# Kernel tuning notes

Measured on AMD Instinct MI355X. Metric: run time of the kernel, lower is better.

Reference implementation:

```python
import jax, jax.numpy as jnp
import numpy as np

DIM = 2048
NUM_HEADS = 16
HEAD_DIM = DIM // NUM_HEADS  # 128
B, T = 2, 2048
ROPE_BASE = 10000.0


def _rope_tables(seq_len, head_dim, dtype=jnp.float32):
    inv_freq = 1.0 / (ROPE_BASE ** (jnp.arange(0, head_dim, 2, dtype=jnp.float32) / head_dim))
    t = jnp.arange(seq_len, dtype=jnp.float32)
    freqs = jnp.einsum('i,j->ij', t, inv_freq)          # [T, head_dim/2]
    emb = jnp.concatenate([freqs, freqs], axis=-1)       # [T, head_dim]
    return jnp.cos(emb).astype(dtype), jnp.sin(emb).astype(dtype)


def _rotate_half(x):
    x1, x2 = jnp.split(x, 2, axis=-1)
    return jnp.concatenate([-x2, x1], axis=-1)


def setup_inputs() -> dict:
    key = jax.random.key(0)
    k1, k2, k3 = jax.random.split(key, 3)
    x = jax.random.normal(k1, (B, T, DIM), dtype=jnp.float32)
    w_qkv = jax.random.normal(k2, (3 * DIM, DIM), dtype=jnp.float32) * (DIM ** -0.5)
    w_out = jax.random.normal(k3, (DIM, DIM), dtype=jnp.float32) * (DIM ** -0.5)
    return {"x": x, "w_qkv": w_qkv, "w_out": w_out}


def reference(x, w_qkv, w_out):
    b, t, _ = x.shape
    scale = HEAD_DIM ** -0.5

    qkv = x @ w_qkv.T                                    # [B, T, 3*dim]
    q, k, v = jnp.split(qkv, 3, axis=-1)
    # [B, H, T, hd]
    q = q.reshape(b, t, NUM_HEADS, HEAD_DIM).transpose(0, 2, 1, 3)
    k = k.reshape(b, t, NUM_HEADS, HEAD_DIM).transpose(0, 2, 1, 3)
    v = v.reshape(b, t, NUM_HEADS, HEAD_DIM).transpose(0, 2, 1, 3)

    cos, sin = _rope_tables(t, HEAD_DIM, x.dtype)        # [T, hd] broadcast over B,H
    q = q * cos + _rotate_half(q) * sin
    k = k * cos + _rotate_half(k) * sin

    scores = jnp.einsum('bhqd,bhkd->bhqk', q, k) * scale  # [B, H, T, T]
    causal = jnp.tril(jnp.ones((t, t), dtype=bool))
    scores = jnp.where(causal, scores, jnp.float32(-jnp.inf).astype(scores.dtype))
    attn = jax.nn.softmax(scores, axis=-1)
    out = jnp.einsum('bhqk,bhkd->bhqd', attn, v)         # [B, H, T, hd]
    out = out.transpose(0, 2, 1, 3).reshape(b, t, DIM)
    out = out @ w_out.T
    return out
```

## Files before the change

### kernel.cpp

```cpp
#include <hip/hip_runtime.h>
#include <hip/hip_bf16.h>
#include <stdint.h>
#include <math.h>

#define DIMC 2048
#define NH 16
#define HD 128
#define BBATCH 2
#define TSEQ 2048
#define MROWS (BBATCH*TSEQ)
#define NQKV (3*DIMC)

typedef __attribute__((ext_vector_type(8))) short short8;
typedef __attribute__((ext_vector_type(4))) float f32x4;

#define BAR() asm volatile("s_barrier" ::: "memory")

__device__ __forceinline__ short f2bf(float f) {
  union { float f; uint32_t u; } v; v.f = f;
  uint32_t r = (v.u + 0x7fffu + ((v.u >> 16) & 1u)) >> 16;
  return (short)(uint16_t)r;
}
__device__ __forceinline__ float bf2f(short s) {
  union { uint32_t u; float f; } v; v.u = ((uint32_t)(uint16_t)s) << 16;
  return v.f;
}
__device__ __forceinline__ void g2lds16(const void* g, void* l) {
  __builtin_amdgcn_global_load_lds((const __attribute__((address_space(1))) void*)g,
                                   (__attribute__((address_space(3))) void*)l, 16, 0, 0);
}

__global__ void rope_tables(float* __restrict__ cos_t, float* __restrict__ sin_t) {
  int idx = blockIdx.x * blockDim.x + threadIdx.x;
  int t = idx >> 6, j = idx & 63;
  double inv = exp(-((double)(2 * j) / 128.0) * log(10000.0));
  float fr = (float)t * (float)inv;
  cos_t[idx] = cosf(fr);
  sin_t[idx] = sinf(fr);
}

__global__ void cast_f32_bf16(const float* __restrict__ in, short* __restrict__ out, int n8) {
  int i = blockIdx.x * blockDim.x + threadIdx.x;
  if (i >= n8) return;
  const float4* p = (const float4*)in;
  float4 a = p[2 * i], b = p[2 * i + 1];
  short8 o;
  o[0] = f2bf(a.x); o[1] = f2bf(a.y); o[2] = f2bf(a.z); o[3] = f2bf(a.w);
  o[4] = f2bf(b.x); o[5] = f2bf(b.y); o[6] = f2bf(b.z); o[7] = f2bf(b.w);
  ((short8*)out)[i] = o;
}

__global__ void rope_apply(short* __restrict__ q, short* __restrict__ k,
                           const float* __restrict__ cos_t, const float* __restrict__ sin_t) {
  int idx = blockIdx.x * blockDim.x + threadIdx.x;
  int j = idx & 63;
  int t = (idx >> 6) & (TSEQ - 1);
  int bh = idx >> 17;
  size_t base = ((size_t)bh * TSEQ + t) * HD;
  float c = cos_t[t * 64 + j], s = sin_t[t * 64 + j];
  float x1 = bf2f(q[base + j]), x2 = bf2f(q[base + j + 64]);
  q[base + j]      = f2bf(x1 * c - x2 * s);
  q[base + j + 64] = f2bf(x2 * c + x1 * s);
  float y1 = bf2f(k[base + j]), y2 = bf2f(k[base + j + 64]);
  k[base + j]      = f2bf(y1 * c - y2 * s);
  k[base + j + 64] = f2bf(y2 * c + y1 * s);
}

__device__ __forceinline__ void stage128(short* lds_base, const short* gsrc, int ldg, int tid) {
  #pragma unroll
  for (int j = 0; j < 2; ++j) {
    int L = j * 512 + tid;
    int r = L >> 3, pc = L & 7;
    g2lds16(gsrc + (size_t)r * ldg + ((pc ^ (r & 7)) << 3), lds_base + L * 8);
  }
}
__device__ __forceinline__ short8 ldsfrag(const short* base, int row, int c) {
  return *(const short8*)(base + row * 64 + ((c ^ (row & 7)) << 3));
}

template<int EPI>
__global__ __launch_bounds__(512, 2)
void gemm256(const short* __restrict__ A, const short* __restrict__ B,
             int M, int N, int K,
             float* __restrict__ Cout,
             short* __restrict__ qp, short* __restrict__ kp, short* __restrict__ vp) {
  __shared__ short Ab[2][256 * 64];
  __shared__ short Bb[3][128 * 64];
  const int tid = threadIdx.x;
  const int lane = tid & 63, wave = tid >> 6;
  const int wm = wave >> 2, wn = wave & 3;
  const int bn = blockIdx.x, bm = blockIdx.y;
  const int rowA0 = bm * 256, rowB0 = bn * 128;
  const int NT = K / 64;
  const int l15 = lane & 15, l4 = lane >> 4;
  f32x4 acc[8][2] = {};

  stage128(&Ab[0][0],        A + (size_t)rowA0 * K,         K, tid);
  stage128(&Ab[0][128 * 64], A + (size_t)(rowA0 + 128) * K, K, tid);
  stage128(&Bb[0][0],        B + (size_t)rowB0 * K,         K, tid);
  stage128(&Bb[1][0],        B + (size_t)rowB0 * K + 64,    K, tid);
  asm volatile("s_waitcnt vmcnt(2)" ::: "memory");
  BAR();

  for (int t = 0; t < NT; ++t) {
    const short* At = Ab[t & 1];
    const short* Bt = Bb[t % 3];
    short* Anx = Ab[(t + 1) & 1];
    short* Bnx = Bb[(t + 2) % 3];
    const short* Ag = A + (size_t)rowA0 * K + (t + 1) * 64;
    const short* Bg = B + (size_t)rowB0 * K + (t + 2) * 64;
    short8 bfrag[2][2];
    #pragma unroll
    for (int ph = 0; ph < 4; ++ph) {
      short8 afrag[2][2];
      if (ph == 0) {
        #pragma unroll
        for (int n = 0; n < 2; ++n)
          #pragma unroll
          for (int ks = 0; ks < 2; ++ks)
            bfrag[n][ks] = ldsfrag(Bt, wn * 32 + n * 16 + l15, ks * 4 + l4);
      }
      #pragma unroll
      for (int m2 = 0; m2 < 2; ++m2)
        #pragma unroll
        for (int ks = 0; ks < 2; ++ks)
          afrag[m2][ks] = ldsfrag(At, wm * 128 + (ph * 2 + m2) * 16 + l15, ks * 4 + l4);
      if (ph == 0 && t + 1 < NT) stage128(Anx,            Ag,                    K, tid);
      if (ph == 1 && t + 1 < NT) stage128(Anx + 128 * 64, Ag + (size_t)128 * K,  K, tid);
      if (ph == 2 && t + 2 < NT) stage128(Bnx,            Bg,                    K, tid);
      if (ph == 3) {
        if (t + 2 < NT) asm volatile("s_waitcnt vmcnt(2)" ::: "memory");
        else            asm volatile("s_waitcnt vmcnt(0)" ::: "memory");
      }
      BAR();
      __builtin_amdgcn_s_setprio(1);
      #pragma unroll
      for (int m2 = 0; m2 < 2; ++m2)
        #pragma unroll
        for (int n = 0; n < 2; ++n)
          #pragma unroll
          for (int ks = 0; ks < 2; ++ks)
            acc[ph * 2 + m2][n] =
                __builtin_amdgcn_mfma_f32_16x16x32_bf16(afrag[m2][ks], bfrag[n][ks],
                                                        acc[ph * 2 + m2][n], 0, 0, 0);
      __builtin_amdgcn_s_setprio(0);
    }
  }

  if (EPI == 1) {
    #pragma unroll
    for (int m = 0; m < 8; ++m)
      #pragma unroll
      for (int n = 0; n < 2; ++n)
        #pragma unroll
        for (int i = 0; i < 4; ++i) {
          int gm = rowA0 + wm * 128 + m * 16 + (l4 << 2) + i;
          int gn = rowB0 + wn * 32 + n * 16 + l15;
          Cout[(size_t)gm * N + gn] = acc[m][n][i];
        }
  } else {
    short* dst = (bn < 16) ? qp : (bn < 32) ? kp : vp;
    int h = bn & 15;
    #pragma unroll
    for (int m = 0; m < 8; ++m)
      #pragma unroll
      for (int n = 0; n < 2; ++n)
        #pragma unroll
        for (int i = 0; i < 4; ++i) {
          int gm = rowA0 + wm * 128 + m * 16 + (l4 << 2) + i;
          int b = gm >> 11, tt = gm & 2047;
          int d = wn * 32 + n * 16 + l15;
          dst[(((size_t)b * NH + h) * TSEQ + tt) * HD + d] = f2bf(acc[m][n][i]);
        }
  }
}

__global__ __launch_bounds__(256)
void flash_attn(const short* __restrict__ Q, const short* __restrict__ K,
                const short* __restrict__ V, short* __restrict__ Oout) {
  __shared__ short Ks[64 * 128];
  __shared__ short Vt[128 * 64];
  __shared__ short Pl[4 * 16 * 64];
  int tid = threadIdx.x, lane = tid & 63, wave = tid >> 6;
  int bid = blockIdx.x;
  int qt = (TSEQ / 64 - 1) - (bid >> 5);
  int hb = bid & 31;
  int h = hb & 15, b = hb >> 4;
  size_t bh_off = ((size_t)b * NH + h) * TSEQ * HD;
  const short* Qp = Q + bh_off;
  const short* Kp = K + bh_off;
  const short* Vp = V + bh_off;
  int q0 = qt * 64 + wave * 16;
  short8 qf[4];
  #pragma unroll
  for (int ks = 0; ks < 4; ++ks)
    qf[ks] = *(const short8*)(Qp + (size_t)(q0 + (lane & 15)) * HD + ks * 32 + 8 * (lane >> 4));
  float m_run[4], l_run[4];
  f32x4 acc_o[8] = {};
  #pragma unroll
  for (int i = 0; i < 4; ++i) { m_run[i] = -INFINITY; l_run[i] = 0.f; }
  const float scale = 0.08838834764831845f;
  for (int it = 0; it <= qt; ++it) {
    int kv0 = it * 64;
    short8 vv[4];
    #pragma unroll
    for (int j = 0; j < 4; ++j) {
      int e = tid + j * 256;
      int r = e >> 4, c0 = (e & 15) * 8;
      vv[j] = *(const short8*)(Vp + (size_t)(kv0 + r) * HD + c0);
    }
    #pragma unroll
    for (int j = 0; j < 4; ++j) {
      int c = tid + j * 256;
      int r = c >> 4, cc = c & 15;
      g2lds16(Kp + (size_t)(kv0 + r) * HD + ((cc ^ (r & 7)) << 3), Ks + c * 8);
    }
    #pragma unroll
    for (int j = 0; j < 4; ++j) {
      int e = tid + j * 256;
      int r = e >> 4, c0 = (e & 15) * 8;
      int rc = r >> 3, rl = r & 7;
      #pragma unroll
      for (int jj = 0; jj < 8; ++jj) {
        int d = c0 + jj;
        int pch = rc ^ (d & 7) ^ ((d >> 3) & 7);
        Vt[d * 64 + (pch << 3) + rl] = vv[j][jj];
      }
    }
    __syncthreads();
    f32x4 sa[4] = {};
    __builtin_amdgcn_s_setprio(1);
    #pragma unroll
    for (int nf = 0; nf < 4; ++nf)
      #pragma unroll
      for (int ks = 0; ks < 4; ++ks) {
        int row = nf * 16 + (lane & 15);
        int lch = ks * 4 + (lane >> 4);
        short8 kf = *(const short8*)(Ks + row * 128 + ((lch ^ (row & 7)) << 3));
        sa[nf] = __builtin_amdgcn_mfma_f32_16x16x32_bf16(qf[ks], kf, sa[nf], 0, 0, 0);
      }
    __builtin_amdgcn_s_setprio(0);
    bool lastTile = (it == qt);
    #pragma unroll
    for (int nf = 0; nf < 4; ++nf)
      #pragma unroll
      for (int i = 0; i < 4; ++i) {
        float s = sa[nf][i] * scale;
        if (lastTile) {
          int kvc = kv0 + nf * 16 + (lane & 15);
          int qr = q0 + ((lane >> 4) << 2) + i;
          if (kvc > qr) s = -INFINITY;
        }
        sa[nf][i] = s;
      }
    #pragma unroll
    for (int i = 0; i < 4; ++i) {
      float t = fmaxf(fmaxf(sa[0][i], sa[1][i]), fmaxf(sa[2][i], sa[3][i]));
      t = fmaxf(t, __shfl_xor(t, 1));
      t = fmaxf(t, __shfl_xor(t, 2));
      t = fmaxf(t, __shfl_xor(t, 4));
      t = fmaxf(t, __shfl_xor(t, 8));
      float mn = fmaxf(m_run[i], t);
      float al = __expf(m_run[i] - mn);
      m_run[i] = mn;
      float su = 0.f;
      #pragma unroll
      for (int nf = 0; nf < 4; ++nf) {
        float p = __expf(sa[nf][i] - mn);
        sa[nf][i] = p;
        su += p;
      }
      su += __shfl_xor(su, 1);
      su += __shfl_xor(su, 2);
      su += __shfl_xor(su, 4);
      su += __shfl_xor(su, 8);
      l_run[i] = l_run[i] * al + su;
      #pragma unroll
      for (int nfd = 0; nfd < 8; ++nfd) acc_o[nfd][i] *= al;
    }
    short* Pw = Pl + wave * 16 * 64;
    #pragma unroll
    for (int nf = 0; nf < 4; ++nf)
      #pragma unroll
      for (int i = 0; i < 4; ++i) {
        int qq = ((lane >> 4) << 2) + i;
        int kv = nf * 16 + (lane & 15);
        Pw[qq * 64 + (((kv >> 3) ^ (qq & 7)) << 3) + (kv & 7)] = f2bf(sa[nf][i]);
      }
    __builtin_amdgcn_s_setprio(1);
    #pragma unroll
    for (int ks2 = 0; ks2 < 2; ++ks2) {
      int qq = lane & 15;
      int lchp = ks2 * 4 + (lane >> 4);
      short8 pf = *(const short8*)(Pw + qq * 64 + ((lchp ^ (qq & 7)) << 3));
      #pragma unroll
      for (int nfd = 0; nfd < 8; ++nfd) {
        int d = nfd * 16 + (lane & 15);
        int lch = ks2 * 4 + (lane >> 4);
        int pch = lch ^ (d & 7) ^ ((d >> 3) & 7);
        short8 vf = *(const short8*)(Vt + d * 64 + (pch << 3));
        acc_o[nfd] = __builtin_amdgcn_mfma_f32_16x16x32_bf16(pf, vf, acc_o[nfd], 0, 0, 0);
      }
    }
    __builtin_amdgcn_s_setprio(0);
    __syncthreads();
  }
  #pragma unroll
  for (int nfd = 0; nfd < 8; ++nfd)
    #pragma unroll
    for (int i = 0; i < 4; ++i) {
      int qr = q0 + ((lane >> 4) << 2) + i;
      int col = h * HD + nfd * 16 + (lane & 15);
      Oout[((size_t)b * TSEQ + qr) * DIMC + col] = f2bf(acc_o[nfd][i] / l_run[i]);
    }
}

extern "C" void kernel_launch(void* const* d_in, const int* in_sizes, int n_in,
                              void* d_out, int out_size, void* d_ws, size_t ws_size,
                              hipStream_t stream) {
  const float* x     = (const float*)d_in[0];
  const float* w_qkv = (const float*)d_in[1];
  const float* w_out = (const float*)d_in[2];
  float* out = (float*)d_out;
  char* ws = (char*)d_ws;
  size_t off = 0;
  auto alloc = [&](size_t bytes) {
    void* p = ws + off;
    off += (bytes + 255) & ~(size_t)255;
    return p;
  };
  float* cos_t = (float*)alloc((size_t)TSEQ * 64 * 4);
  float* sin_t = (float*)alloc((size_t)TSEQ * 64 * 4);
  short* xb    = (short*)alloc((size_t)MROWS * DIMC * 2);
  short* wqkvb = (short*)alloc((size_t)NQKV * DIMC * 2);
  short* woutb = (short*)alloc((size_t)DIMC * DIMC * 2);
  short* q     = (short*)alloc((size_t)BBATCH * NH * TSEQ * HD * 2);
  short* k     = (short*)alloc((size_t)BBATCH * NH * TSEQ * HD * 2);
  short* v     = (short*)alloc((size_t)BBATCH * NH * TSEQ * HD * 2);
  short* attn  = (short*)alloc((size_t)MROWS * DIMC * 2);

  rope_tables<<<(TSEQ * 64) / 256, 256, 0, stream>>>(cos_t, sin_t);
  cast_f32_bf16<<<(MROWS * DIMC / 8 + 255) / 256, 256, 0, stream>>>(x, xb, MROWS * DIMC / 8);
  cast_f32_bf16<<<(NQKV * DIMC / 8 + 255) / 256, 256, 0, stream>>>(w_qkv, wqkvb, NQKV * DIMC / 8);
  cast_f32_bf16<<<(DIMC * DIMC / 8 + 255) / 256, 256, 0, stream>>>(w_out, woutb, DIMC * DIMC / 8);

  gemm256<0><<<dim3(NQKV / 128, MROWS / 256), 512, 0, stream>>>(
      xb, wqkvb, MROWS, NQKV, DIMC, nullptr, q, k, v);

  rope_apply<<<(BBATCH * NH * TSEQ * 64) / 256, 256, 0, stream>>>(q, k, cos_t, sin_t);

  flash_attn<<<dim3((TSEQ / 64) * NH * BBATCH), 256, 0, stream>>>(q, k, v, attn);

  gemm256<1><<<dim3(DIMC / 128, MROWS / 256), 512, 0, stream>>>(
      attn, woutb, MROWS, DIMC, DIMC, out, nullptr, nullptr, nullptr);
}
```

Measured before the change: 447.1 us.

## Enlarge GEMM tiles to 256x256 with quadrant-pipelined loads and swizzled block order

The GEMM kernel now computes 256x256 output tiles instead of 256x128. Each wave holds a 128x64 accumulator, A and B are double-buffered in 128-row LDS halves, and global-to-LDS staging is interleaved with four MFMA quadrant phases per k-step. Workgroup indices are remapped in groups of 8 to improve L2 locality. This raises arithmetic intensity and cuts redundant A reloads, at the cost of more registers per thread and half as many workgroups, which may reduce occupancy and tail balance. The QKV epilogue now derives the head from the column index.

```diff
diff --git a/kernel.cpp b/kernel.cpp
--- a/kernel.cpp
+++ b/kernel.cpp
@@ -78,98 +78,139 @@
   return *(const short8*)(base + row * 64 + ((c ^ (row & 7)) << 3));
 }
 
+template<int Q>
+__device__ __forceinline__ void mfma16(short8 (&afr)[8][2], short8 (&bfr)[4][2],
+                                       f32x4 (&acc)[8][4]) {
+  constexpr int rh = Q >> 1, ch = Q & 1;
+  #pragma unroll
+  for (int m2 = 0; m2 < 4; ++m2)
+    #pragma unroll
+    for (int n2 = 0; n2 < 2; ++n2)
+      #pragma unroll
+      for (int ks = 0; ks < 2; ++ks)
+        acc[rh * 4 + m2][ch * 2 + n2] = __builtin_amdgcn_mfma_f32_16x16x32_bf16(
+            afr[rh * 4 + m2][ks], bfr[ch * 2 + n2][ks], acc[rh * 4 + m2][ch * 2 + n2], 0, 0, 0);
+}
+template<int H>
+__device__ __forceinline__ void loads_half(short8 (&afr)[8][2], short8 (&bfr)[4][2],
+                                           const short* Acur, const short* Bcur,
+                                           int brow, int l15, int l4) {
+  #pragma unroll
+  for (int m2 = 0; m2 < 4; ++m2)
+    #pragma unroll
+    for (int ks = 0; ks < 2; ++ks)
+      afr[H * 4 + m2][ks] = ldsfrag(Acur, H * 64 + m2 * 16 + l15, ks * 4 + l4);
+  #pragma unroll
+  for (int n2 = 0; n2 < 2; ++n2)
+    #pragma unroll
+    for (int ks = 0; ks < 2; ++ks)
+      bfr[H * 2 + n2][ks] = ldsfrag(Bcur, brow + H * 32 + n2 * 16 + l15, ks * 4 + l4);
+}
+
 template<int EPI>
 __global__ __launch_bounds__(512, 2)
 void gemm256(const short* __restrict__ A, const short* __restrict__ B,
              int M, int N, int K,
              float* __restrict__ Cout,
              short* __restrict__ qp, short* __restrict__ kp, short* __restrict__ vp) {
-  __shared__ short Ab[2][256 * 64];
-  __shared__ short Bb[3][128 * 64];
-  const int tid = threadIdx.x;
-  const int lane = tid & 63, wave = tid >> 6;
+  __shared__ short Asl[2][2][128 * 64];
+  __shared__ short Bsl[2][2][128 * 64];
+  const int tid = threadIdx.x, lane = tid & 63, wave = tid >> 6;
   const int wm = wave >> 2, wn = wave & 3;
-  const int bn = blockIdx.x, bm = blockIdx.y;
-  const int rowA0 = bm * 256, rowB0 = bn * 128;
+  const int l15 = lane & 15, l4 = lane >> 4;
+  const int nwg = gridDim.x * gridDim.y;
+  const int orig = blockIdx.y * gridDim.x + blockIdx.x;
+  const int wg = (orig & 7) * (nwg >> 3) + (orig >> 3);
+  const int bn = wg % gridDim.x, bm = wg / gridDim.x;
+  const int rowA0 = bm * 256, rowB0 = bn * 256;
   const int NT = K / 64;
-  const int l15 = lane & 15, l4 = lane >> 4;
-  f32x4 acc[8][2] = {};
-
-  stage128(&Ab[0][0],        A + (size_t)rowA0 * K,         K, tid);
-  stage128(&Ab[0][128 * 64], A + (size_t)(rowA0 + 128) * K, K, tid);
-  stage128(&Bb[0][0],        B + (size_t)rowB0 * K,         K, tid);
-  stage128(&Bb[1][0],        B + (size_t)rowB0 * K + 64,    K, tid);
-  asm volatile("s_waitcnt vmcnt(2)" ::: "memory");
+  f32x4 acc[8][4] = {};
+  short8 afr[8][2], bfr[4][2];
+
+  auto stA = [&](int kt, int h) {
+    if (kt < NT) stage128(&Asl[kt & 1][h][0], A + (size_t)(rowA0 + h * 128) * K + kt * 64, K, tid);
+  };
+  auto stB = [&](int kt, int h) {
+    if (kt < NT) stage128(&Bsl[kt & 1][h][0], B + (size_t)(rowB0 + h * 128) * K + kt * 64, K, tid);
+  };
+
+  stA(0, 0); stA(0, 1); stB(0, 0); stB(0, 1); stA(1, 0); stA(1, 1);
+  asm volatile("s_waitcnt vmcnt(4)" ::: "memory");
   BAR();
 
-  for (int t = 0; t < NT; ++t) {
-    const short* At = Ab[t & 1];
-    const short* Bt = Bb[t % 3];
-    short* Anx = Ab[(t + 1) & 1];
-    short* Bnx = Bb[(t + 2) % 3];
-    const short* Ag = A + (size_t)rowA0 * K + (t + 1) * 64;
-    const short* Bg = B + (size_t)rowB0 * K + (t + 2) * 64;
-    short8 bfrag[2][2];
-    #pragma unroll
-    for (int ph = 0; ph < 4; ++ph) {
-      short8 afrag[2][2];
-      if (ph == 0) {
-        #pragma unroll
-        for (int n = 0; n < 2; ++n)
-          #pragma unroll
-          for (int ks = 0; ks < 2; ++ks)
-            bfrag[n][ks] = ldsfrag(Bt, wn * 32 + n * 16 + l15, ks * 4 + l4);
-      }
-      #pragma unroll
-      for (int m2 = 0; m2 < 2; ++m2)
-        #pragma unroll
-        for (int ks = 0; ks < 2; ++ks)
-          afrag[m2][ks] = ldsfrag(At, wm * 128 + (ph * 2 + m2) * 16 + l15, ks * 4 + l4);
-      if (ph == 0 && t + 1 < NT) stage128(Anx,            Ag,                    K, tid);
-      if (ph == 1 && t + 1 < NT) stage128(Anx + 128 * 64, Ag + (size_t)128 * K,  K, tid);
-      if (ph == 2 && t + 2 < NT) stage128(Bnx,            Bg,                    K, tid);
-      if (ph == 3) {
-        if (t + 2 < NT) asm volatile("s_waitcnt vmcnt(2)" ::: "memory");
-        else            asm volatile("s_waitcnt vmcnt(0)" ::: "memory");
-      }
-      BAR();
-      __builtin_amdgcn_s_setprio(1);
-      #pragma unroll
-      for (int m2 = 0; m2 < 2; ++m2)
-        #pragma unroll
-        for (int n = 0; n < 2; ++n)
-          #pragma unroll
-          for (int ks = 0; ks < 2; ++ks)
-            acc[ph * 2 + m2][n] =
-                __builtin_amdgcn_mfma_f32_16x16x32_bf16(afrag[m2][ks], bfrag[n][ks],
-                                                        acc[ph * 2 + m2][n], 0, 0, 0);
-      __builtin_amdgcn_s_setprio(0);
-    }
+  const short* A0 = &Asl[0][wm][0];
+  const short* B0 = &Bsl[0][wn >> 1][0];
+  const short* A1 = &Asl[1][wm][0];
+  const short* B1 = &Bsl[1][wn >> 1][0];
+  const int brow = (wn & 1) * 64;
+
+  for (int t = 0; t < NT / 2; ++t) {
+    const int k0 = 2 * t, k1 = 2 * t + 1;
+    const bool lastIt = (t == NT / 2 - 1);
+    loads_half<0>(afr, bfr, A0, B0, brow, l15, l4);
+    stB(k1, 0);
+    BAR();
+    __builtin_amdgcn_s_setprio(1); mfma16<0>(afr, bfr, acc); __builtin_amdgcn_s_setprio(0);
+    BAR();
+    loads_half<1>(afr, bfr, A0, B0, brow, l15, l4);
+    stB(k1, 1);
+    BAR();
+    __builtin_amdgcn_s_setprio(1); mfma16<1>(afr, bfr, acc); __builtin_amdgcn_s_setprio(0);
+    BAR();
+    stA(k0 + 2, 0);
+    BAR();
+    __builtin_amdgcn_s_setprio(1); mfma16<2>(afr, bfr, acc); __builtin_amdgcn_s_setprio(0);
+    BAR();
+    stA(k0 + 2, 1);
+    if (lastIt) asm volatile("s_waitcnt vmcnt(0)" ::: "memory");
+    else        asm volatile("s_waitcnt vmcnt(4)" ::: "memory");
+    BAR();
+    __builtin_amdgcn_s_setprio(1); mfma16<3>(afr, bfr, acc); __builtin_amdgcn_s_setprio(0);
+    BAR();
+    loads_half<0>(afr, bfr, A1, B1, brow, l15, l4);
+    stB(k0 + 2, 0);
+    BAR();
+    __builtin_amdgcn_s_setprio(1); mfma16<0>(afr, bfr, acc); __builtin_amdgcn_s_setprio(0);
+    BAR();
+    loads_half<1>(afr, bfr, A1, B1, brow, l15, l4);
+    stB(k0 + 2, 1);
+    BAR();
+    __builtin_amdgcn_s_setprio(1); mfma16<1>(afr, bfr, acc); __builtin_amdgcn_s_setprio(0);
+    BAR();
+    stA(k1 + 2, 0);
+    BAR();
+    __builtin_amdgcn_s_setprio(1); mfma16<2>(afr, bfr, acc); __builtin_amdgcn_s_setprio(0);
+    BAR();
+    stA(k1 + 2, 1);
+    if (!lastIt) asm volatile("s_waitcnt vmcnt(4)" ::: "memory");
+    BAR();
+    __builtin_amdgcn_s_setprio(1); mfma16<3>(afr, bfr, acc); __builtin_amdgcn_s_setprio(0);
+    BAR();
   }
 
   if (EPI == 1) {
     #pragma unroll
     for (int m = 0; m < 8; ++m)
       #pragma unroll
-      for (int n = 0; n < 2; ++n)
+      for (int n = 0; n < 4; ++n)
         #pragma unroll
         for (int i = 0; i < 4; ++i) {
-          int gm = rowA0 + wm * 128 + m * 16 + (l4 << 2) + i;
-          int gn = rowB0 + wn * 32 + n * 16 + l15;
+          int gm = rowA0 + wm * 128 + (m >> 2) * 64 + (m & 3) * 16 + (l4 << 2) + i;
+          int gn = rowB0 + wn * 64 + (n >> 1) * 32 + (n & 1) * 16 + l15;
           Cout[(size_t)gm * N + gn] = acc[m][n][i];
         }
   } else {
-    short* dst = (bn < 16) ? qp : (bn < 32) ? kp : vp;
-    int h = bn & 15;
+    short* dst = (bn < 8) ? qp : (bn < 16) ? kp : vp;
     #pragma unroll
     for (int m = 0; m < 8; ++m)
       #pragma unroll
-      for (int n = 0; n < 2; ++n)
+      for (int n = 0; n < 4; ++n)
         #pragma unroll
         for (int i = 0; i < 4; ++i) {
-          int gm = rowA0 + wm * 128 + m * 16 + (l4 << 2) + i;
+          int gm = rowA0 + wm * 128 + (m >> 2) * 64 + (m & 3) * 16 + (l4 << 2) + i;
+          int c  = rowB0 + wn * 64 + (n >> 1) * 32 + (n & 1) * 16 + l15;
           int b = gm >> 11, tt = gm & 2047;
-          int d = wn * 32 + n * 16 + l15;
+          int h = (c >> 7) & 15, d = c & 127;
           dst[(((size_t)b * NH + h) * TSEQ + tt) * HD + d] = f2bf(acc[m][n][i]);
         }
   }
@@ -344,13 +385,13 @@
   cast_f32_bf16<<<(NQKV * DIMC / 8 + 255) / 256, 256, 0, stream>>>(w_qkv, wqkvb, NQKV * DIMC / 8);
   cast_f32_bf16<<<(DIMC * DIMC / 8 + 255) / 256, 256, 0, stream>>>(w_out, woutb, DIMC * DIMC / 8);
 
-  gemm256<0><<<dim3(NQKV / 128, MROWS / 256), 512, 0, stream>>>(
+  gemm256<0><<<dim3(NQKV / 256, MROWS / 256), 512, 0, stream>>>(
       xb, wqkvb, MROWS, NQKV, DIMC, nullptr, q, k, v);
 
   rope_apply<<<(BBATCH * NH * TSEQ * 64) / 256, 256, 0, stream>>>(q, k, cos_t, sin_t);
 
   flash_attn<<<dim3((TSEQ / 64) * NH * BBATCH), 256, 0, stream>>>(q, k, v, attn);
 
-  gemm256<1><<<dim3(DIMC / 128, MROWS / 256), 512, 0, stream>>>(
+  gemm256<1><<<dim3(DIMC / 256, MROWS / 256), 512, 0, stream>>>(
       attn, woutb, MROWS, DIMC, DIMC, out, nullptr, nullptr, nullptr);
 }
```

Result: no change. 448.6 us (+0.4%).
